# Performance work log

Measured on AMD Instinct MI355X. Metric: run time of the kernel, lower is better.

The kernel has to match this reference:

```python
import jax, jax.numpy as jnp
import numpy as np

MARGIN = 1.0


def setup_inputs() -> dict:
    key = jax.random.key(0)
    k1, k2, k3 = jax.random.split(key, 3)
    N, F = 4096, 512
    a = jax.random.normal(k1, (N, F), dtype=jnp.float32)
    b = jax.random.normal(k2, (N, F), dtype=jnp.float32)
    labels = jax.random.randint(k3, (N,), 0, 16, dtype=jnp.int32)
    return {"a": a, "b": b, "labels": labels}


def reference(a, b, labels):
    # D[i, j] = ||b_i - a_j||  (torch: Xa=a[None], Xb=b[:,None], sum over feat)
    # GEMM form of the pairwise sqdist; clamp tiny fp negatives before sqrt.
    Dsq = (jnp.sum(b * b, axis=1)[:, None]
           + jnp.sum(a * a, axis=1)[None, :]
           - 2.0 * (b @ a.T))
    D = jnp.sqrt(jnp.maximum(Dsq, 0.0))            # [N, N]
    Dexpm = jnp.exp(MARGIN - D)                    # [N, N]

    same = labels[:, None] == labels[None, :]      # [N, N]
    eye = jnp.eye(labels.shape[0], dtype=bool)
    pos_mask = same & ~eye                         # ordered positive pairs (i, j)
    neg_mask = ~same                               # negative pairs (labels differ)

    # neg_i sum for row i: sum_k Dexpm[i, k] over k with labels[k] != labels[i]
    row_negsum = jnp.sum(jnp.where(neg_mask, Dexpm, 0.0), axis=1)  # [N]

    # J_ij = log(neg_ik_sum + neg_jl_sum) + D[i, j]; hinged and squared
    J = jnp.log(row_negsum[:, None] + row_negsum[None, :]) + D
    hinge_sq = jnp.square(jnp.maximum(J, 0.0))

    num_pos = jnp.sum(pos_mask)
    return jnp.sum(jnp.where(pos_mask, hinge_sq, 0.0)) / (2.0 * num_pos)
```

## Files before the change

kernel.cpp:

```cpp
#include <hip/hip_runtime.h>
#include <math.h>

#define NROW 4096
#define FDIM 512
#define MARGIN 1.0f
#define NLAB 16
#define PREP_BLK 1024

typedef __attribute__((ext_vector_type(8))) short short8;
typedef __attribute__((ext_vector_type(4))) float floatx4;

__device__ inline unsigned short f2bf(float x) {
    unsigned u = __float_as_uint(x);
    return (unsigned short)((u + 0x7FFFu + ((u >> 16) & 1u)) >> 16);
}
__device__ inline void glds16(const unsigned short* g, unsigned short* l) {
    __builtin_amdgcn_global_load_lds(
        (const __attribute__((address_space(1))) unsigned int*)g,
        (__attribute__((address_space(3))) unsigned int*)l, 16, 0, 0);
}
#define WAIT_VM_BARRIER(N)                                          \
    do {                                                            \
        asm volatile("s_waitcnt vmcnt(" #N ")" ::: "memory");       \
        __builtin_amdgcn_s_barrier();                               \
        __builtin_amdgcn_sched_barrier(0);                          \
    } while (0)

__device__ inline float fast_sqrt_pos(float dsq) {
    float c = fmaxf(dsq, 1e-20f);
    return c * __frsqrt_rn(c);
}

__global__ __launch_bounds__(256) void prep_kernel(
    const float* __restrict__ a, const float* __restrict__ b,
    const int* __restrict__ labels,
    unsigned short* __restrict__ abf, unsigned short* __restrict__ bbf,
    float* __restrict__ na, float* __restrict__ nb,
    float* __restrict__ rns, float* __restrict__ loss,
    int* __restrict__ perm, int* __restrict__ goff,
    int* __restrict__ wl, int* __restrict__ wlmeta) {
    const int t = threadIdx.x;

    if (blockIdx.x == PREP_BLK) {
        __shared__ int hist[NLAB], off[NLAB], cur[NLAB];
        if (t < NLAB) hist[t] = 0;
        __syncthreads();
        for (int i = t; i < NROW; i += 256) atomicAdd(&hist[labels[i] & 15], 1);
        __syncthreads();
        if (t == 0) {
            int acc = 0;
            for (int g = 0; g < NLAB; ++g) { off[g] = acc; acc += hist[g]; }
            int n = 0;
            long long np = 0;
            for (int g = 0; g < NLAB; ++g) {
                goff[g] = off[g];
                int c = hist[g];
                np += (long long)c * (long long)(c - 1);
                int nt = (c + 63) >> 6;
                for (int ti = 0; ti < nt; ++ti)
                    for (int tj = 0; tj < nt; ++tj)
                        wl[n++] = (g << 12) | (ti << 6) | tj;
            }
            goff[NLAB] = NROW;
            wlmeta[0] = n;
            wlmeta[1] = (int)np;
            wlmeta[2] = 0;
            loss[0]   = 0.f;
        }
        __syncthreads();
        if (t < NLAB) cur[t] = off[t];
        __syncthreads();
        for (int i = t; i < NROW; i += 256) {
            int pos = atomicAdd(&cur[labels[i] & 15], 1);
            perm[pos] = i;
        }
        return;
    }

    const int grp = t >> 6;
    const int ln  = t & 63;
    const int row = blockIdx.x * 4 + grp;
    const float4* a4 = (const float4*)(a + (size_t)row * FDIM);
    const float4* b4 = (const float4*)(b + (size_t)row * FDIM);
    const int f = ln * 2;
    float4 va0 = a4[f], va1 = a4[f + 1];
    float4 vb0 = b4[f], vb1 = b4[f + 1];
    float sa = va0.x * va0.x + va0.y * va0.y + va0.z * va0.z + va0.w * va0.w
             + va1.x * va1.x + va1.y * va1.y + va1.z * va1.z + va1.w * va1.w;
    float sb = vb0.x * vb0.x + vb0.y * vb0.y + vb0.z * vb0.z + vb0.w * vb0.w
             + vb1.x * vb1.x + vb1.y * vb1.y + vb1.z * vb1.z + vb1.w * vb1.w;
    short8 ua, ub;
    ua[0] = (short)f2bf(va0.x); ua[1] = (short)f2bf(va0.y);
    ua[2] = (short)f2bf(va0.z); ua[3] = (short)f2bf(va0.w);
    ua[4] = (short)f2bf(va1.x); ua[5] = (short)f2bf(va1.y);
    ua[6] = (short)f2bf(va1.z); ua[7] = (short)f2bf(va1.w);
    ub[0] = (short)f2bf(vb0.x); ub[1] = (short)f2bf(vb0.y);
    ub[2] = (short)f2bf(vb0.z); ub[3] = (short)f2bf(vb0.w);
    ub[4] = (short)f2bf(vb1.x); ub[5] = (short)f2bf(vb1.y);
    ub[6] = (short)f2bf(vb1.z); ub[7] = (short)f2bf(vb1.w);
    *(short8*)&abf[(size_t)row * FDIM + (size_t)f * 4] = ua;
    *(short8*)&bbf[(size_t)row * FDIM + (size_t)f * 4] = ub;
    #pragma unroll
    for (int o = 32; o > 0; o >>= 1) {
        sa += __shfl_down(sa, o);
        sb += __shfl_down(sb, o);
    }
    if (ln == 0) {
        na[row] = sa;
        nb[row] = sb;
        rns[row] = 0.f;
    }
}

__global__ __launch_bounds__(512, 2) void pass_neg(
    const unsigned short* __restrict__ abf, const unsigned short* __restrict__ bbf,
    const int* __restrict__ labels,
    const float* __restrict__ na, const float* __restrict__ nb,
    float* __restrict__ rns)
{
    __shared__ __align__(16) unsigned short arena[65536];
    __shared__ float rpart[4][256];

    const int t    = threadIdx.x;
    const int lane = t & 63;
    const int w    = t >> 6;
    const int wi   = w >> 2;
    const int wj   = w & 3;
    const int lr   = lane & 15;
    const int lq   = lane >> 4;

    const int bid = blockIdx.x;
    const int wg  = (bid & 7) * 32 + (bid >> 3);
    const int by  = wg >> 4, bx = wg & 15;
    const int ti  = by * 256;
    const int tj  = bx * 256;

    floatx4 acc[8][4];
    #pragma unroll
    for (int i = 0; i < 8; ++i)
        #pragma unroll
        for (int j = 0; j < 4; ++j)
            acc[i][j] = (floatx4){0.f, 0.f, 0.f, 0.f};

    auto stage = [&](int kk, int buf) {
        unsigned short* As = arena + buf * 16384;
        unsigned short* Bs = As + 8192;
        #pragma unroll
        for (int l = 0; l < 2; ++l) {
            int c   = t + l * 512;
            int row = c >> 2;
            int qs  = (c & 3) ^ ((row >> 1) & 3);
            glds16(abf + (size_t)(tj + row) * FDIM + kk + qs * 8, As + c * 8);
            glds16(bbf + (size_t)(ti + row) * FDIM + kk + qs * 8, Bs + c * 8);
        }
    };

    stage(0, 0);
    stage(32, 1);
    stage(64, 2);
    WAIT_VM_BARRIER(8);

    #pragma unroll
    for (int it = 0; it < 16; ++it) {
        if (it < 13) stage((it + 3) * 32, (it + 3) & 3);

        const unsigned short* As = arena + (it & 3) * 16384;
        const unsigned short* Bs = As + 8192;
        short8 af[8], bv[4];
        #pragma unroll
        for (int ri = 0; ri < 8; ++ri) {
            int R = wi * 128 + ri * 16 + lr;
            af[ri] = *(const short8*)
                &Bs[R * 32 + ((lq ^ ((R >> 1) & 3))) * 8];
        }
        #pragma unroll
        for (int rj = 0; rj < 4; ++rj) {
            int R = wj * 64 + rj * 16 + lr;
            bv[rj] = *(const short8*)
                &As[R * 32 + ((lq ^ ((R >> 1) & 3))) * 8];
        }
        __builtin_amdgcn_s_setprio(1);
        #pragma unroll
        for (int ri = 0; ri < 8; ++ri)
            #pragma unroll
            for (int rj = 0; rj < 4; ++rj)
                acc[ri][rj] = __builtin_amdgcn_mfma_f32_16x16x32_bf16(
                    af[ri], bv[rj], acc[ri][rj], 0, 0, 0);
        __builtin_amdgcn_s_setprio(0);

        if (it < 13) {
            WAIT_VM_BARRIER(8);
        } else if (it == 13) {
            WAIT_VM_BARRIER(4);
        } else if (it == 14) {
            WAIT_VM_BARRIER(0);
        }
    }

    int   ljv[4]; float najv[4];
    #pragma unroll
    for (int rj = 0; rj < 4; ++rj) {
        int jl = wj * 64 + rj * 16 + lr;
        ljv[rj]  = labels[tj + jl];
        najv[rj] = na[tj + jl];
    }
    #pragma unroll
    for (int ri = 0; ri < 8; ++ri) {
        float rs[4] = {0.f, 0.f, 0.f, 0.f};
        int liv[4]; float nbv[4];
        #pragma unroll
        for (int r = 0; r < 4; ++r) {
            int il = wi * 128 + ri * 16 + lq * 4 + r;
            liv[r] = labels[ti + il];
            nbv[r] = nb[ti + il];
        }
        #pragma unroll
        for (int rj = 0; rj < 4; ++rj)
            #pragma unroll
            for (int r = 0; r < 4; ++r) {
                float dsq  = nbv[r] + najv[rj] - 2.f * acc[ri][rj][r];
                float D    = fast_sqrt_pos(dsq);
                float mask = (liv[r] != ljv[rj]) ? 1.f : 0.f;
                rs[r] = fmaf(mask, __expf(MARGIN - D), rs[r]);
            }
        #pragma unroll
        for (int r = 0; r < 4; ++r) {
            #pragma unroll
            for (int o = 8; o > 0; o >>= 1) rs[r] += __shfl_down(rs[r], o, 16);
        }
        if (lr == 0) {
            #pragma unroll
            for (int r = 0; r < 4; ++r)
                rpart[wj][wi * 128 + ri * 16 + lq * 4 + r] = rs[r];
        }
    }
    __syncthreads();
    if (t < 256) {
        float s = rpart[0][t] + rpart[1][t] + rpart[2][t] + rpart[3][t];
        atomicAdd(&rns[ti + t], s);
    }
}

__global__ __launch_bounds__(256) void pass2_pos(
    const unsigned short* __restrict__ abf, const unsigned short* __restrict__ bbf,
    const float* __restrict__ na, const float* __restrict__ nb,
    const float* __restrict__ rns,
    const int* __restrict__ perm, const int* __restrict__ goff,
    const int* __restrict__ wl, const int* __restrict__ wlmeta,
    float* __restrict__ loss_sum, int* __restrict__ done,
    float* __restrict__ out)
{
    __shared__ __align__(16) unsigned short arena[32768];
    __shared__ int   rows_i[64], rows_j[64];
    __shared__ float rbi_s[64], rbj_s[64], nbi_s[64], naj_s[64];
    __shared__ float part[4];

    const int t    = threadIdx.x;
    const int lane = t & 63;
    const int w    = t >> 6;
    const int wi   = w >> 1, wj = w & 1;
    const int lr   = lane & 15;
    const int lq   = lane >> 4;
    const int nwl  = wlmeta[0];

    float local = 0.f;

    for (int item = blockIdx.x; item < nwl; item += gridDim.x) {
        __syncthreads();
        int e  = wl[item];
        int g  = e >> 12, ti = (e >> 6) & 63, tj = e & 63;
        int gb = goff[g], ge = goff[g + 1];
        int cnt = ge - gb;

        if (t < 64) {
            int idx = gb + ti * 64 + t;
            int ig  = perm[idx < ge ? idx : gb];
            rows_i[t] = ig;
            rbi_s[t]  = rns[ig];
            nbi_s[t]  = nb[ig];
        } else if (t < 128) {
            int u   = t - 64;
            int idx = gb + tj * 64 + u;
            int jg  = perm[idx < ge ? idx : gb];
            rows_j[u] = jg;
            rbj_s[u]  = rns[jg];
            naj_s[u]  = na[jg];
        }
        __syncthreads();

        floatx4 acc[2][2];
        #pragma unroll
        for (int i = 0; i < 2; ++i)
            #pragma unroll
            for (int j = 0; j < 2; ++j)
                acc[i][j] = (floatx4){0.f, 0.f, 0.f, 0.f};

        auto stage = [&](int kk, int buf) {
            unsigned short* As = arena + buf * 16384;
            unsigned short* Bs = As + 8192;
            #pragma unroll
            for (int l = 0; l < 4; ++l) {
                int c   = t + l * 256;
                int row = c >> 4;
                int qs  = (c & 15) ^ (row & 7);
                glds16(abf + (size_t)rows_j[row] * FDIM + kk + qs * 8,
                       As + c * 8);
                glds16(bbf + (size_t)rows_i[row] * FDIM + kk + qs * 8,
                       Bs + c * 8);
            }
        };

        stage(0, 0);
        WAIT_VM_BARRIER(0);

        #pragma unroll
        for (int itk = 0; itk < 4; ++itk) {
            if (itk < 3) stage((itk + 1) * 128, (itk + 1) & 1);

            const unsigned short* As = arena + (itk & 1) * 16384;
            const unsigned short* Bs = As + 8192;
            #pragma unroll
            for (int ks = 0; ks < 4; ++ks) {
                short8 af[2], bfv[2];
                #pragma unroll
                for (int ri = 0; ri < 2; ++ri) {
                    int R = wi * 32 + ri * 16 + lr;
                    af[ri] = *(const short8*)
                        &Bs[R * 128 + (((ks * 4 + lq) ^ (R & 7))) * 8];
                }
                #pragma unroll
                for (int rj = 0; rj < 2; ++rj) {
                    int R = wj * 32 + rj * 16 + lr;
                    bfv[rj] = *(const short8*)
                        &As[R * 128 + (((ks * 4 + lq) ^ (R & 7))) * 8];
                }
                #pragma unroll
                for (int ri = 0; ri < 2; ++ri)
                    #pragma unroll
                    for (int rj = 0; rj < 2; ++rj)
                        acc[ri][rj] = __builtin_amdgcn_mfma_f32_16x16x32_bf16(
                            af[ri], bfv[rj], acc[ri][rj], 0, 0, 0);
            }
            if (itk < 3) WAIT_VM_BARRIER(0);
        }

        #pragma unroll
        for (int ri = 0; ri < 2; ++ri)
            #pragma unroll
            for (int rj = 0; rj < 2; ++rj) {
                int  jl  = wj * 32 + rj * 16 + lr;
                bool vj  = (tj * 64 + jl) < cnt;
                int  jg  = rows_j[jl];
                float nav = naj_s[jl], rbj = rbj_s[jl];
                #pragma unroll
                for (int r = 0; r < 4; ++r) {
                    int  il = wi * 32 + ri * 16 + lq * 4 + r;
                    bool vi = (ti * 64 + il) < cnt;
                    if (vi && vj && rows_i[il] != jg) {
                        float dsq = nbi_s[il] + nav - 2.f * acc[ri][rj][r];
                        float D   = fast_sqrt_pos(dsq);
                        float J   = __logf(rbi_s[il] + rbj) + D;
                        float h   = fmaxf(J, 0.f);
                        local += h * h;
                    }
                }
            }
    }

    #pragma unroll
    for (int o = 32; o > 0; o >>= 1) local += __shfl_down(local, o);
    if (lane == 0) part[w] = local;
    __syncthreads();
    if (t == 0) {
        atomicAdd(loss_sum, part[0] + part[1] + part[2] + part[3]);
        __threadfence();
        int old = atomicAdd(done, 1);
        if (old == (int)gridDim.x - 1) {
            __threadfence();
            float total = *(volatile float*)loss_sum;
            out[0] = total / (2.0f * (float)wlmeta[1]);
        }
    }
}

extern "C" void kernel_launch(void* const* d_in, const int* in_sizes, int n_in,
                              void* d_out, int out_size, void* d_ws, size_t ws_size,
                              hipStream_t stream) {
    const float* a      = (const float*)d_in[0];
    const float* b      = (const float*)d_in[1];
    const int*   labels = (const int*)d_in[2];
    float* out = (float*)d_out;

    unsigned short* abf = (unsigned short*)d_ws;
    unsigned short* bbf = abf + (size_t)NROW * FDIM;
    float* fws  = (float*)(bbf + (size_t)NROW * FDIM);
    float* na   = fws;
    float* nb   = fws + NROW;
    float* rns  = fws + 2 * NROW;
    float* loss = fws + 3 * NROW;
    int* iws    = (int*)(fws + 3 * NROW + 4);
    int* perm   = iws;
    int* goff   = iws + NROW;
    int* wlmeta = iws + NROW + 20;
    int* wl     = iws + NROW + 24;

    prep_kernel<<<PREP_BLK + 1, 256, 0, stream>>>(a, b, labels, abf, bbf,
                                                  na, nb, rns, loss,
                                                  perm, goff, wl, wlmeta);
    pass_neg<<<(NROW / 256) * (NROW / 256), 512, 0, stream>>>(abf, bbf, labels,
                                                              na, nb, rns);
    pass2_pos<<<384, 256, 0, stream>>>(abf, bbf, na, nb, rns, perm, goff, wl,
                                       wlmeta, loss, &wlmeta[2], out);
}
```

Baseline: 123.2 us.

## Remap neg-pass tiles per XCD, stage two k-steps per barrier, load full K in pos pass

```diff
diff --git a/kernel.cpp b/kernel.cpp
--- a/kernel.cpp
+++ b/kernel.cpp
@@ -130,8 +130,9 @@
     const int lq   = lane >> 4;
 
     const int bid = blockIdx.x;
-    const int wg  = (bid & 7) * 32 + (bid >> 3);
-    const int by  = wg >> 4, bx = wg & 15;
+    const int xcd = bid & 7, loc = bid >> 3;
+    const int by  = (xcd >> 1) * 4 + (loc >> 3);
+    const int bx  = (xcd & 1) * 8 + (loc & 7);
     const int ti  = by * 256;
     const int tj  = bx * 256;
 
@@ -142,9 +143,10 @@
         for (int j = 0; j < 4; ++j)
             acc[i][j] = (floatx4){0.f, 0.f, 0.f, 0.f};
 
-    auto stage = [&](int kk, int buf) {
-        unsigned short* As = arena + buf * 16384;
+    auto stage = [&](int s) {
+        unsigned short* As = arena + (s & 3) * 16384;
         unsigned short* Bs = As + 8192;
+        const int kk = s * 32;
         #pragma unroll
         for (int l = 0; l < 2; ++l) {
             int c   = t + l * 512;
@@ -155,46 +157,43 @@
         }
     };
 
-    stage(0, 0);
-    stage(32, 1);
-    stage(64, 2);
-    WAIT_VM_BARRIER(8);
-
-    #pragma unroll
-    for (int it = 0; it < 16; ++it) {
-        if (it < 13) stage((it + 3) * 32, (it + 3) & 3);
-
-        const unsigned short* As = arena + (it & 3) * 16384;
-        const unsigned short* Bs = As + 8192;
-        short8 af[8], bv[4];
-        #pragma unroll
-        for (int ri = 0; ri < 8; ++ri) {
-            int R = wi * 128 + ri * 16 + lr;
-            af[ri] = *(const short8*)
-                &Bs[R * 32 + ((lq ^ ((R >> 1) & 3))) * 8];
-        }
-        #pragma unroll
-        for (int rj = 0; rj < 4; ++rj) {
-            int R = wj * 64 + rj * 16 + lr;
-            bv[rj] = *(const short8*)
-                &As[R * 32 + ((lq ^ ((R >> 1) & 3))) * 8];
-        }
-        __builtin_amdgcn_s_setprio(1);
-        #pragma unroll
-        for (int ri = 0; ri < 8; ++ri)
-            #pragma unroll
-            for (int rj = 0; rj < 4; ++rj)
-                acc[ri][rj] = __builtin_amdgcn_mfma_f32_16x16x32_bf16(
-                    af[ri], bv[rj], acc[ri][rj], 0, 0, 0);
-        __builtin_amdgcn_s_setprio(0);
-
-        if (it < 13) {
-            WAIT_VM_BARRIER(8);
-        } else if (it == 13) {
-            WAIT_VM_BARRIER(4);
-        } else if (it == 14) {
-            WAIT_VM_BARRIER(0);
-        }
+    stage(0);
+    stage(1);
+    WAIT_VM_BARRIER(0);
+
+    #pragma unroll
+    for (int p = 0; p < 8; ++p) {
+        if (p < 7) { stage(2 * p + 2); stage(2 * p + 3); }
+
+        #pragma unroll
+        for (int ss = 0; ss < 2; ++ss) {
+            const int s = 2 * p + ss;
+            const unsigned short* As = arena + (s & 3) * 16384;
+            const unsigned short* Bs = As + 8192;
+            short8 af[8], bv[4];
+            #pragma unroll
+            for (int ri = 0; ri < 8; ++ri) {
+                int R = wi * 128 + ri * 16 + lr;
+                af[ri] = *(const short8*)
+                    &Bs[R * 32 + ((lq ^ ((R >> 1) & 3))) * 8];
+            }
+            #pragma unroll
+            for (int rj = 0; rj < 4; ++rj) {
+                int R = wj * 64 + rj * 16 + lr;
+                bv[rj] = *(const short8*)
+                    &As[R * 32 + ((lq ^ ((R >> 1) & 3))) * 8];
+            }
+            __builtin_amdgcn_s_setprio(1);
+            #pragma unroll
+            for (int ri = 0; ri < 8; ++ri)
+                #pragma unroll
+                for (int rj = 0; rj < 4; ++rj)
+                    acc[ri][rj] = __builtin_amdgcn_mfma_f32_16x16x32_bf16(
+                        af[ri], bv[rj], acc[ri][rj], 0, 0, 0);
+            __builtin_amdgcn_s_setprio(0);
+        }
+
+        if (p < 7) WAIT_VM_BARRIER(0);
     }
 
     int   ljv[4]; float najv[4];
@@ -250,7 +249,7 @@
     float* __restrict__ loss_sum, int* __restrict__ done,
     float* __restrict__ out)
 {
-    __shared__ __align__(16) unsigned short arena[32768];
+    __shared__ __align__(16) unsigned short arena[65536];
     __shared__ int   rows_i[64], rows_j[64];
     __shared__ float rbi_s[64], rbj_s[64], nbi_s[64], naj_s[64];
     __shared__ float part[4];
@@ -288,6 +287,17 @@
         }
         __syncthreads();
 
+        #pragma unroll
+        for (int l = 0; l < 16; ++l) {
+            int c   = t + l * 256;
+            int row = c >> 6;
+            int qs  = (c & 63) ^ (row & 7);
+            glds16(abf + (size_t)rows_j[row] * FDIM + qs * 8, arena + c * 8);
+            glds16(bbf + (size_t)rows_i[row] * FDIM + qs * 8,
+                   arena + 32768 + c * 8);
+        }
+        WAIT_VM_BARRIER(0);
+
         floatx4 acc[2][2];
         #pragma unroll
         for (int i = 0; i < 2; ++i)
@@ -295,53 +305,29 @@
             for (int j = 0; j < 2; ++j)
                 acc[i][j] = (floatx4){0.f, 0.f, 0.f, 0.f};
 
-        auto stage = [&](int kk, int buf) {
-            unsigned short* As = arena + buf * 16384;
-            unsigned short* Bs = As + 8192;
-            #pragma unroll
-            for (int l = 0; l < 4; ++l) {
-                int c   = t + l * 256;
-                int row = c >> 4;
-                int qs  = (c & 15) ^ (row & 7);
-                glds16(abf + (size_t)rows_j[row] * FDIM + kk + qs * 8,
-                       As + c * 8);
-                glds16(bbf + (size_t)rows_i[row] * FDIM + kk + qs * 8,
-                       Bs + c * 8);
-            }
-        };
-
-        stage(0, 0);
-        WAIT_VM_BARRIER(0);
-
-        #pragma unroll
-        for (int itk = 0; itk < 4; ++itk) {
-            if (itk < 3) stage((itk + 1) * 128, (itk + 1) & 1);
-
-            const unsigned short* As = arena + (itk & 1) * 16384;
-            const unsigned short* Bs = As + 8192;
-            #pragma unroll
-            for (int ks = 0; ks < 4; ++ks) {
-                short8 af[2], bfv[2];
+        const unsigned short* As = arena;
+        const unsigned short* Bs = arena + 32768;
+        #pragma unroll
+        for (int ks = 0; ks < 16; ++ks) {
+            short8 af[2], bfv[2];
+            #pragma unroll
+            for (int ri = 0; ri < 2; ++ri) {
+                int R  = wi * 32 + ri * 16 + lr;
+                int cs = (ks * 4 + lq) ^ (R & 7);
+                af[ri] = *(const short8*)&Bs[R * 512 + cs * 8];
+            }
+            #pragma unroll
+            for (int rj = 0; rj < 2; ++rj) {
+                int R  = wj * 32 + rj * 16 + lr;
+                int cs = (ks * 4 + lq) ^ (R & 7);
+                bfv[rj] = *(const short8*)&As[R * 512 + cs * 8];
+            }
+            #pragma unroll
+            for (int ri = 0; ri < 2; ++ri)
                 #pragma unroll
-                for (int ri = 0; ri < 2; ++ri) {
-                    int R = wi * 32 + ri * 16 + lr;
-                    af[ri] = *(const short8*)
-                        &Bs[R * 128 + (((ks * 4 + lq) ^ (R & 7))) * 8];
-                }
-                #pragma unroll
-                for (int rj = 0; rj < 2; ++rj) {
-                    int R = wj * 32 + rj * 16 + lr;
-                    bfv[rj] = *(const short8*)
-                        &As[R * 128 + (((ks * 4 + lq) ^ (R & 7))) * 8];
-                }
-                #pragma unroll
-                for (int ri = 0; ri < 2; ++ri)
-                    #pragma unroll
-                    for (int rj = 0; rj < 2; ++rj)
-                        acc[ri][rj] = __builtin_amdgcn_mfma_f32_16x16x32_bf16(
-                            af[ri], bfv[rj], acc[ri][rj], 0, 0, 0);
-            }
-            if (itk < 3) WAIT_VM_BARRIER(0);
+                for (int rj = 0; rj < 2; ++rj)
+                    acc[ri][rj] = __builtin_amdgcn_mfma_f32_16x16x32_bf16(
+                        af[ri], bfv[rj], acc[ri][rj], 0, 0, 0);
         }
 
         #pragma unroll
@@ -409,6 +395,6 @@
                                                   perm, goff, wl, wlmeta);
     pass_neg<<<(NROW / 256) * (NROW / 256), 512, 0, stream>>>(abf, bbf, labels,
                                                               na, nb, rns);
-    pass2_pos<<<384, 256, 0, stream>>>(abf, bbf, na, nb, rns, perm, goff, wl,
+    pass2_pos<<<256, 256, 0, stream>>>(abf, bbf, na, nb, rns, perm, goff, wl,
                                        wlmeta, loss, &wlmeta[2], out);
 }
```

Measured after the change: 130.1 us. 5.6% more time.

## Fuse negative-sum and positive-pair passes into one persistent kernel with grid barrier

Applied to the files above, without the earlier changes.

```diff
diff --git a/kernel.cpp b/kernel.cpp
--- a/kernel.cpp
+++ b/kernel.cpp
@@ -6,6 +6,7 @@
 #define MARGIN 1.0f
 #define NLAB 16
 #define PREP_BLK 1024
+#define NBLK 256
 
 typedef __attribute__((ext_vector_type(8))) short short8;
 typedef __attribute__((ext_vector_type(4))) float floatx4;
@@ -29,6 +30,18 @@
 __device__ inline float fast_sqrt_pos(float dsq) {
     float c = fmaxf(dsq, 1e-20f);
     return c * __frsqrt_rn(c);
+}
+
+__device__ inline void grid_sync(int* bar) {
+    __syncthreads();
+    if (threadIdx.x == 0) {
+        __threadfence();
+        atomicAdd(bar, 1);
+        while (__hip_atomic_load(bar, __ATOMIC_RELAXED,
+                                 __HIP_MEMORY_SCOPE_AGENT) < NBLK)
+            __builtin_amdgcn_s_sleep(1);
+    }
+    __syncthreads();
 }
 
 __global__ __launch_bounds__(256) void prep_kernel(
@@ -65,6 +78,7 @@
             wlmeta[0] = n;
             wlmeta[1] = (int)np;
             wlmeta[2] = 0;
+            wlmeta[3] = 0;
             loss[0]   = 0.f;
         }
         __syncthreads();
@@ -112,252 +126,241 @@
     }
 }
 
-__global__ __launch_bounds__(512, 2) void pass_neg(
+__global__ __launch_bounds__(512, 2) void negpos_kernel(
     const unsigned short* __restrict__ abf, const unsigned short* __restrict__ bbf,
     const int* __restrict__ labels,
     const float* __restrict__ na, const float* __restrict__ nb,
-    float* __restrict__ rns)
+    float* __restrict__ rns,
+    const int* __restrict__ perm, const int* __restrict__ goff,
+    const int* __restrict__ wl, int* __restrict__ wlmeta,
+    float* __restrict__ loss_sum, float* __restrict__ out)
 {
     __shared__ __align__(16) unsigned short arena[65536];
     __shared__ float rpart[4][256];
+    __shared__ int   rows_i[64], rows_j[64];
+    __shared__ float rbi_s[64], rbj_s[64], nbi_s[64], naj_s[64];
+    __shared__ float part[8];
 
     const int t    = threadIdx.x;
     const int lane = t & 63;
     const int w    = t >> 6;
-    const int wi   = w >> 2;
-    const int wj   = w & 3;
     const int lr   = lane & 15;
     const int lq   = lane >> 4;
-
-    const int bid = blockIdx.x;
-    const int wg  = (bid & 7) * 32 + (bid >> 3);
-    const int by  = wg >> 4, bx = wg & 15;
-    const int ti  = by * 256;
-    const int tj  = bx * 256;
-
-    floatx4 acc[8][4];
-    #pragma unroll
-    for (int i = 0; i < 8; ++i)
+    const int bid  = blockIdx.x;
+
+    {
+        const int wi = w >> 2;
+        const int wj = w & 3;
+
+        const int wg = (bid & 7) * 32 + (bid >> 3);
+        const int by = wg >> 4, bx = wg & 15;
+        const int ti = by * 256;
+        const int tj = bx * 256;
+
+        floatx4 acc[8][4];
         #pragma unroll
-        for (int j = 0; j < 4; ++j)
-            acc[i][j] = (floatx4){0.f, 0.f, 0.f, 0.f};
-
-    auto stage = [&](int kk, int buf) {
-        unsigned short* As = arena + buf * 16384;
-        unsigned short* Bs = As + 8192;
+        for (int i = 0; i < 8; ++i)
+            #pragma unroll
+            for (int j = 0; j < 4; ++j)
+                acc[i][j] = (floatx4){0.f, 0.f, 0.f, 0.f};
+
+        auto stage = [&](int s) {
+            unsigned short* As = arena + (s & 3) * 16384;
+            unsigned short* Bs = As + 8192;
+            const int kk = s * 32;
+            #pragma unroll
+            for (int l = 0; l < 2; ++l) {
+                int c   = t + l * 512;
+                int row = c >> 2;
+                int qs  = (c & 3) ^ ((row >> 1) & 3);
+                glds16(abf + (size_t)(tj + row) * FDIM + kk + qs * 8, As + c * 8);
+                glds16(bbf + (size_t)(ti + row) * FDIM + kk + qs * 8, Bs + c * 8);
+            }
+        };
+
+        stage(0);
+        stage(1);
+        stage(2);
+        WAIT_VM_BARRIER(8);
+
         #pragma unroll
-        for (int l = 0; l < 2; ++l) {
-            int c   = t + l * 512;
-            int row = c >> 2;
-            int qs  = (c & 3) ^ ((row >> 1) & 3);
-            glds16(abf + (size_t)(tj + row) * FDIM + kk + qs * 8, As + c * 8);
-            glds16(bbf + (size_t)(ti + row) * FDIM + kk + qs * 8, Bs + c * 8);
-        }
-    };
-
-    stage(0, 0);
-    stage(32, 1);
-    stage(64, 2);
-    WAIT_VM_BARRIER(8);
-
-    #pragma unroll
-    for (int it = 0; it < 16; ++it) {
-        if (it < 13) stage((it + 3) * 32, (it + 3) & 3);
-
-        const unsigned short* As = arena + (it & 3) * 16384;
-        const unsigned short* Bs = As + 8192;
-        short8 af[8], bv[4];
+        for (int it = 0; it < 16; ++it) {
+            if (it < 13) stage(it + 3);
+
+            const unsigned short* As = arena + (it & 3) * 16384;
+            const unsigned short* Bs = As + 8192;
+            short8 af[8], bv[4];
+            #pragma unroll
+            for (int ri = 0; ri < 8; ++ri) {
+                int R = wi * 128 + ri * 16 + lr;
+                af[ri] = *(const short8*)
+                    &Bs[R * 32 + ((lq ^ ((R >> 1) & 3))) * 8];
+            }
+            #pragma unroll
+            for (int rj = 0; rj < 4; ++rj) {
+                int R = wj * 64 + rj * 16 + lr;
+                bv[rj] = *(const short8*)
+                    &As[R * 32 + ((lq ^ ((R >> 1) & 3))) * 8];
+            }
+            __builtin_amdgcn_s_setprio(1);
+            #pragma unroll
+            for (int ri = 0; ri < 8; ++ri)
+                #pragma unroll
+                for (int rj = 0; rj < 4; ++rj)
+                    acc[ri][rj] = __builtin_amdgcn_mfma_f32_16x16x32_bf16(
+                        af[ri], bv[rj], acc[ri][rj], 0, 0, 0);
+            __builtin_amdgcn_s_setprio(0);
+
+            if (it < 13) {
+                WAIT_VM_BARRIER(8);
+            } else if (it == 13) {
+                WAIT_VM_BARRIER(4);
+            } else if (it == 14) {
+                WAIT_VM_BARRIER(0);
+            }
+        }
+
+        int   ljv[4]; float najv[4];
+        #pragma unroll
+        for (int rj = 0; rj < 4; ++rj) {
+            int jl = wj * 64 + rj * 16 + lr;
+            ljv[rj]  = labels[tj + jl];
+            najv[rj] = na[tj + jl];
+        }
         #pragma unroll
         for (int ri = 0; ri < 8; ++ri) {
-            int R = wi * 128 + ri * 16 + lr;
-            af[ri] = *(const short8*)
-                &Bs[R * 32 + ((lq ^ ((R >> 1) & 3))) * 8];
-        }
-        #pragma unroll
-        for (int rj = 0; rj < 4; ++rj) {
-            int R = wj * 64 + rj * 16 + lr;
-            bv[rj] = *(const short8*)
-                &As[R * 32 + ((lq ^ ((R >> 1) & 3))) * 8];
-        }
-        __builtin_amdgcn_s_setprio(1);
-        #pragma unroll
-        for (int ri = 0; ri < 8; ++ri)
+            float rs[4] = {0.f, 0.f, 0.f, 0.f};
+            int liv[4]; float nbv[4];
+            #pragma unroll
+            for (int r = 0; r < 4; ++r) {
+                int il = wi * 128 + ri * 16 + lq * 4 + r;
+                liv[r] = labels[ti + il];
+                nbv[r] = nb[ti + il];
+            }
             #pragma unroll
             for (int rj = 0; rj < 4; ++rj)
-                acc[ri][rj] = __builtin_amdgcn_mfma_f32_16x16x32_bf16(
-                    af[ri], bv[rj], acc[ri][rj], 0, 0, 0);
-        __builtin_amdgcn_s_setprio(0);
-
-        if (it < 13) {
-            WAIT_VM_BARRIER(8);
-        } else if (it == 13) {
-            WAIT_VM_BARRIER(4);
-        } else if (it == 14) {
+                #pragma unroll
+                for (int r = 0; r < 4; ++r) {
+                    float dsq  = nbv[r] + najv[rj] - 2.f * acc[ri][rj][r];
+                    float D    = fast_sqrt_pos(dsq);
+                    float mask = (liv[r] != ljv[rj]) ? 1.f : 0.f;
+                    rs[r] = fmaf(mask, __expf(MARGIN - D), rs[r]);
+                }
+            #pragma unroll
+            for (int r = 0; r < 4; ++r) {
+                #pragma unroll
+                for (int o = 8; o > 0; o >>= 1)
+                    rs[r] += __shfl_down(rs[r], o, 16);
+            }
+            if (lr == 0) {
+                #pragma unroll
+                for (int r = 0; r < 4; ++r)
+                    rpart[wj][wi * 128 + ri * 16 + lq * 4 + r] = rs[r];
+            }
+        }
+        __syncthreads();
+        if (t < 256) {
+            float s = rpart[0][t] + rpart[1][t] + rpart[2][t] + rpart[3][t];
+            atomicAdd(&rns[ti + t], s);
+        }
+    }
+
+    grid_sync(&wlmeta[3]);
+
+    {
+        const int wi  = w >> 2;
+        const int wj  = w & 3;
+        const int nwl = wlmeta[0];
+
+        float local = 0.f;
+
+        for (int item = bid; item < nwl; item += NBLK) {
+            __syncthreads();
+            int e  = wl[item];
+            int g  = e >> 12, ti = (e >> 6) & 63, tj = e & 63;
+            int gb = goff[g], ge = goff[g + 1];
+            int cnt = ge - gb;
+
+            if (t < 64) {
+                int idx = gb + ti * 64 + t;
+                int ig  = perm[idx < ge ? idx : gb];
+                rows_i[t] = ig;
+                rbi_s[t]  = __hip_atomic_load(&rns[ig], __ATOMIC_RELAXED,
+                                              __HIP_MEMORY_SCOPE_AGENT);
+                nbi_s[t]  = nb[ig];
+            } else if (t < 128) {
+                int u   = t - 64;
+                int idx = gb + tj * 64 + u;
+                int jg  = perm[idx < ge ? idx : gb];
+                rows_j[u] = jg;
+                rbj_s[u]  = __hip_atomic_load(&rns[jg], __ATOMIC_RELAXED,
+                                              __HIP_MEMORY_SCOPE_AGENT);
+                naj_s[u]  = na[jg];
+            }
+            __syncthreads();
+
+            auto stageP = [&](int kk, int buf) {
+                unsigned short* As = arena + buf * 32768;
+                unsigned short* Bs = As + 16384;
+                #pragma unroll
+                for (int l = 0; l < 4; ++l) {
+                    int c   = t + l * 512;
+                    int row = c >> 5;
+                    int qs  = (c & 31) ^ (row & 7);
+                    glds16(abf + (size_t)rows_j[row] * FDIM + kk + qs * 8,
+                           As + c * 8);
+                    glds16(bbf + (size_t)rows_i[row] * FDIM + kk + qs * 8,
+                           Bs + c * 8);
+                }
+            };
+
+            floatx4 acc[2];
+            acc[0] = (floatx4){0.f, 0.f, 0.f, 0.f};
+            acc[1] = (floatx4){0.f, 0.f, 0.f, 0.f};
+
+            stageP(0, 0);
             WAIT_VM_BARRIER(0);
-        }
-    }
-
-    int   ljv[4]; float najv[4];
-    #pragma unroll
-    for (int rj = 0; rj < 4; ++rj) {
-        int jl = wj * 64 + rj * 16 + lr;
-        ljv[rj]  = labels[tj + jl];
-        najv[rj] = na[tj + jl];
-    }
-    #pragma unroll
-    for (int ri = 0; ri < 8; ++ri) {
-        float rs[4] = {0.f, 0.f, 0.f, 0.f};
-        int liv[4]; float nbv[4];
-        #pragma unroll
-        for (int r = 0; r < 4; ++r) {
-            int il = wi * 128 + ri * 16 + lq * 4 + r;
-            liv[r] = labels[ti + il];
-            nbv[r] = nb[ti + il];
-        }
-        #pragma unroll
-        for (int rj = 0; rj < 4; ++rj)
-            #pragma unroll
-            for (int r = 0; r < 4; ++r) {
-                float dsq  = nbv[r] + najv[rj] - 2.f * acc[ri][rj][r];
-                float D    = fast_sqrt_pos(dsq);
-                float mask = (liv[r] != ljv[rj]) ? 1.f : 0.f;
-                rs[r] = fmaf(mask, __expf(MARGIN - D), rs[r]);
-            }
-        #pragma unroll
-        for (int r = 0; r < 4; ++r) {
-            #pragma unroll
-            for (int o = 8; o > 0; o >>= 1) rs[r] += __shfl_down(rs[r], o, 16);
-        }
-        if (lr == 0) {
-            #pragma unroll
-            for (int r = 0; r < 4; ++r)
-                rpart[wj][wi * 128 + ri * 16 + lq * 4 + r] = rs[r];
-        }
-    }
-    __syncthreads();
-    if (t < 256) {
-        float s = rpart[0][t] + rpart[1][t] + rpart[2][t] + rpart[3][t];
-        atomicAdd(&rns[ti + t], s);
-    }
-}
-
-__global__ __launch_bounds__(256) void pass2_pos(
-    const unsigned short* __restrict__ abf, const unsigned short* __restrict__ bbf,
-    const float* __restrict__ na, const float* __restrict__ nb,
-    const float* __restrict__ rns,
-    const int* __restrict__ perm, const int* __restrict__ goff,
-    const int* __restrict__ wl, const int* __restrict__ wlmeta,
-    float* __restrict__ loss_sum, int* __restrict__ done,
-    float* __restrict__ out)
-{
-    __shared__ __align__(16) unsigned short arena[32768];
-    __shared__ int   rows_i[64], rows_j[64];
-    __shared__ float rbi_s[64], rbj_s[64], nbi_s[64], naj_s[64];
-    __shared__ float part[4];
-
-    const int t    = threadIdx.x;
-    const int lane = t & 63;
-    const int w    = t >> 6;
-    const int wi   = w >> 1, wj = w & 1;
-    const int lr   = lane & 15;
-    const int lq   = lane >> 4;
-    const int nwl  = wlmeta[0];
-
-    float local = 0.f;
-
-    for (int item = blockIdx.x; item < nwl; item += gridDim.x) {
-        __syncthreads();
-        int e  = wl[item];
-        int g  = e >> 12, ti = (e >> 6) & 63, tj = e & 63;
-        int gb = goff[g], ge = goff[g + 1];
-        int cnt = ge - gb;
-
-        if (t < 64) {
-            int idx = gb + ti * 64 + t;
-            int ig  = perm[idx < ge ? idx : gb];
-            rows_i[t] = ig;
-            rbi_s[t]  = rns[ig];
-            nbi_s[t]  = nb[ig];
-        } else if (t < 128) {
-            int u   = t - 64;
-            int idx = gb + tj * 64 + u;
-            int jg  = perm[idx < ge ? idx : gb];
-            rows_j[u] = jg;
-            rbj_s[u]  = rns[jg];
-            naj_s[u]  = na[jg];
-        }
-        __syncthreads();
-
-        floatx4 acc[2][2];
-        #pragma unroll
-        for (int i = 0; i < 2; ++i)
-            #pragma unroll
-            for (int j = 0; j < 2; ++j)
-                acc[i][j] = (floatx4){0.f, 0.f, 0.f, 0.f};
-
-        auto stage = [&](int kk, int buf) {
-            unsigned short* As = arena + buf * 16384;
-            unsigned short* Bs = As + 8192;
-            #pragma unroll
-            for (int l = 0; l < 4; ++l) {
-                int c   = t + l * 256;
-                int row = c >> 4;
-                int qs  = (c & 15) ^ (row & 7);
-                glds16(abf + (size_t)rows_j[row] * FDIM + kk + qs * 8,
-                       As + c * 8);
-                glds16(bbf + (size_t)rows_i[row] * FDIM + kk + qs * 8,
-                       Bs + c * 8);
-            }
-        };
-
-        stage(0, 0);
-        WAIT_VM_BARRIER(0);
-
-        #pragma unroll
-        for (int itk = 0; itk < 4; ++itk) {
-            if (itk < 3) stage((itk + 1) * 128, (itk + 1) & 1);
-
-            const unsigned short* As = arena + (itk & 1) * 16384;
-            const unsigned short* Bs = As + 8192;
-            #pragma unroll
-            for (int ks = 0; ks < 4; ++ks) {
-                short8 af[2], bfv[2];
-                #pragma unroll
-                for (int ri = 0; ri < 2; ++ri) {
-                    int R = wi * 32 + ri * 16 + lr;
-                    af[ri] = *(const short8*)
-                        &Bs[R * 128 + (((ks * 4 + lq) ^ (R & 7))) * 8];
+
+            #pragma unroll
+            for (int itk = 0; itk < 2; ++itk) {
+                if (itk == 0) stageP(256, 1);
+
+                const unsigned short* As = arena + itk * 32768;
+                const unsigned short* Bs = As + 16384;
+                #pragma unroll
+                for (int ks = 0; ks < 8; ++ks) {
+                    short8 af[2], bv;
+                    #pragma unroll
+                    for (int ri = 0; ri < 2; ++ri) {
+                        int R  = wi * 32 + ri * 16 + lr;
+                        int cs = (ks * 4 + lq) ^ (R & 7);
+                        af[ri] = *(const short8*)&Bs[R * 256 + cs * 8];
+                    }
+                    {
+                        int R  = wj * 16 + lr;
+                        int cs = (ks * 4 + lq) ^ (R & 7);
+                        bv = *(const short8*)&As[R * 256 + cs * 8];
+                    }
+                    #pragma unroll
+                    for (int ri = 0; ri < 2; ++ri)
+                        acc[ri] = __builtin_amdgcn_mfma_f32_16x16x32_bf16(
+                            af[ri], bv, acc[ri], 0, 0, 0);
                 }
-                #pragma unroll
-                for (int rj = 0; rj < 2; ++rj) {
-                    int R = wj * 32 + rj * 16 + lr;
-                    bfv[rj] = *(const short8*)
-                        &As[R * 128 + (((ks * 4 + lq) ^ (R & 7))) * 8];
-                }
-                #pragma unroll
-                for (int ri = 0; ri < 2; ++ri)
-                    #pragma unroll
-                    for (int rj = 0; rj < 2; ++rj)
-                        acc[ri][rj] = __builtin_amdgcn_mfma_f32_16x16x32_bf16(
-                            af[ri], bfv[rj], acc[ri][rj], 0, 0, 0);
-            }
-            if (itk < 3) WAIT_VM_BARRIER(0);
-        }
-
-        #pragma unroll
-        for (int ri = 0; ri < 2; ++ri)
-            #pragma unroll
-            for (int rj = 0; rj < 2; ++rj) {
-                int  jl  = wj * 32 + rj * 16 + lr;
-                bool vj  = (tj * 64 + jl) < cnt;
-                int  jg  = rows_j[jl];
-                float nav = naj_s[jl], rbj = rbj_s[jl];
+                if (itk == 0) WAIT_VM_BARRIER(0);
+            }
+
+            int  jl  = wj * 16 + lr;
+            bool vj  = (tj * 64 + jl) < cnt;
+            int  jg  = rows_j[jl];
+            float nav = naj_s[jl], rbj = rbj_s[jl];
+            #pragma unroll
+            for (int ri = 0; ri < 2; ++ri) {
                 #pragma unroll
                 for (int r = 0; r < 4; ++r) {
                     int  il = wi * 32 + ri * 16 + lq * 4 + r;
                     bool vi = (ti * 64 + il) < cnt;
                     if (vi && vj && rows_i[il] != jg) {
-                        float dsq = nbi_s[il] + nav - 2.f * acc[ri][rj][r];
+                        float dsq = nbi_s[il] + nav - 2.f * acc[ri][r];
                         float D   = fast_sqrt_pos(dsq);
                         float J   = __logf(rbi_s[il] + rbj) + D;
                         float h   = fmaxf(J, 0.f);
@@ -365,20 +368,24 @@
                     }
                 }
             }
-    }
-
-    #pragma unroll
-    for (int o = 32; o > 0; o >>= 1) local += __shfl_down(local, o);
-    if (lane == 0) part[w] = local;
-    __syncthreads();
-    if (t == 0) {
-        atomicAdd(loss_sum, part[0] + part[1] + part[2] + part[3]);
-        __threadfence();
-        int old = atomicAdd(done, 1);
-        if (old == (int)gridDim.x - 1) {
+        }
+
+        #pragma unroll
+        for (int o = 32; o > 0; o >>= 1) local += __shfl_down(local, o);
+        if (lane == 0) part[w] = local;
+        __syncthreads();
+        if (t == 0) {
+            float s = 0.f;
+            #pragma unroll
+            for (int i = 0; i < 8; ++i) s += part[i];
+            atomicAdd(loss_sum, s);
             __threadfence();
-            float total = *(volatile float*)loss_sum;
-            out[0] = total / (2.0f * (float)wlmeta[1]);
+            int old = atomicAdd(&wlmeta[2], 1);
+            if (old == NBLK - 1) {
+                __threadfence();
+                float total = *(volatile float*)loss_sum;
+                out[0] = total / (2.0f * (float)wlmeta[1]);
+            }
         }
     }
 }
@@ -407,8 +414,6 @@
     prep_kernel<<<PREP_BLK + 1, 256, 0, stream>>>(a, b, labels, abf, bbf,
                                                   na, nb, rns, loss,
                                                   perm, goff, wl, wlmeta);
-    pass_neg<<<(NROW / 256) * (NROW / 256), 512, 0, stream>>>(abf, bbf, labels,
-                                                              na, nb, rns);
-    pass2_pos<<<384, 256, 0, stream>>>(abf, bbf, na, nb, rns, perm, goff, wl,
-                                       wlmeta, loss, &wlmeta[2], out);
-}
+    negpos_kernel<<<NBLK, 512, 0, stream>>>(abf, bbf, labels, na, nb, rns,
+                                            perm, goff, wl, wlmeta, loss, out);
+}
```

Result: slower. 135.6 us (+10.0%).
